# Optimization experiments

Hardware: AMD Instinct MI355X
Metric: run time of the kernel (lower is better)

## Reference

```python
import jax, jax.numpy as jnp
import numpy as np

B, N, N_HEAD, HDIM = 16, 512, 8, 64


def setup_inputs() -> dict:
    key = jax.random.key(0)
    kq, kk, kv, kg = jax.random.split(key, 4)
    q = jax.random.normal(kq, (B, N, N_HEAD, HDIM), dtype=jnp.float32)
    k = jax.random.normal(kk, (B, N, N_HEAD, HDIM), dtype=jnp.float32)
    v = jax.random.normal(kv, (B, N, N_HEAD, HDIM), dtype=jnp.float32)
    geo_f = jax.random.normal(kg, (B, N, N), dtype=jnp.float32)
    return {"q": q, "k": k, "v": v, "geo_f": geo_f}


def reference(q, k, v, geo_f):
    # q,k,v: [B,N,H,D]; geo_f: [B,N,N]
    D = q.shape[-1]
    scale = D ** (-0.5)  # total_weight = qk_weight / scale  (i.e. * sqrt(D))
    # pairwise_distance = negative squared Euclidean distance between per-head
    # query/key vectors: -||q_i - k_j||^2 = 2 q.k - ||q||^2 - ||k||^2
    qk = jnp.einsum('bnhd,bmhd->bhnm', q, k)            # [B,H,N,N]
    q2 = jnp.sum(q * q, axis=-1).transpose(0, 2, 1)     # [B,H,N]
    k2 = jnp.sum(k * k, axis=-1).transpose(0, 2, 1)     # [B,H,N]
    dist = 2.0 * qk - q2[..., :, None] - k2[..., None, :]
    total = (dist + geo_f[:, None, :, :]) / scale       # geo bias broadcast over heads
    # global max subtraction in the source is a no-op under softmax; softmax is stable anyway
    w = jax.nn.softmax(total, axis=-1)                  # [B,H,N,N]
    # weighted sum over keys m (dropout p=0.0 -> identity)
    out = jnp.einsum('bmhd,bhnm->bnhd', v, w)           # [B,N,H,D]
    return out
```

## Files before the change

### kernel.cpp

```cpp
#include <hip/hip_runtime.h>
#include <hip/hip_bf16.h>

#define BB 16
#define NN 512
#define NH 8
#define DD 64
#define CK 64
#define NCH 8
#define TL 4
#define MWAVES 8
#define MQBLK 128
#define QBLK 64
#define WAVES 4
#define KBLK 128
#define NCHUNK 4
#define NT 32
#define TPC 8

typedef __attribute__((ext_vector_type(8))) short bf16x8;
typedef __attribute__((ext_vector_type(4))) float f32x4;

__device__ __forceinline__ unsigned short f2bf(float f) {
    unsigned int u = __float_as_uint(f);
    u += 0x7fffu + ((u >> 16) & 1u);
    return (unsigned short)(u >> 16);
}
__device__ __forceinline__ float bf2f(unsigned short h) {
    return __uint_as_float(((unsigned int)h) << 16);
}
__device__ __forceinline__ void gload16(const void* gsrc, void* lds) {
    __builtin_amdgcn_global_load_lds(
        (const __attribute__((address_space(1))) unsigned int*)gsrc,
        (__attribute__((address_space(3))) unsigned int*)lds, 16, 0, 0);
}

__global__ __launch_bounds__(256) void geo_prep(
    const float* __restrict__ K, const float* __restrict__ V,
    unsigned short* __restrict__ KhiG, unsigned short* __restrict__ KloG,
    unsigned short* __restrict__ VtG, float* __restrict__ k2G)
{
    const int c2 = blockIdx.x;
    const int h  = blockIdx.y;
    const int b  = blockIdx.z;
    const int bh = b*NH + h;
    const int tid = threadIdx.x;
    const int lane16 = tid & 15;
    const int grp    = tid >> 4;

    __shared__ unsigned short Vl[DD*66];

    const size_t kbase = (size_t)bh*(NN*DD) + (size_t)c2*(CK*DD);
    #pragma unroll
    for (int kk = 0; kk < 4; ++kk) {
        const int kl = kk*16 + grp;
        const float* krow = K + ((size_t)(((b*NN + c2*CK + kl)*NH) + h))*DD + lane16*4;
        const float* vrow = V + ((size_t)(((b*NN + c2*CK + kl)*NH) + h))*DD + lane16*4;
        float4 kf = *(const float4*)krow;
        float4 vf = *(const float4*)vrow;
        float fb[4] = {kf.x, kf.y, kf.z, kf.w};
        float vb[4] = {vf.x, vf.y, vf.z, vf.w};
        unsigned short hu[4], lu[4];
        float k2s = 0.f;
        #pragma unroll
        for (int e = 0; e < 4; ++e) {
            float f = fb[e];
            k2s += f*f;
            hu[e] = f2bf(f);
            lu[e] = f2bf(f - bf2f(hu[e]));
            Vl[(lane16*4 + e)*66 + kl] = f2bf(vb[e]);
        }
        k2s += __shfl_xor(k2s, 1);
        k2s += __shfl_xor(k2s, 2);
        k2s += __shfl_xor(k2s, 4);
        k2s += __shfl_xor(k2s, 8);
        if (lane16 == 0) k2G[bh*NN + c2*CK + kl] = k2s;
        const int pos = (kl*DD + lane16*4) ^ ((kl & 7) << 3);
        *(uint2*)&KhiG[kbase + pos] = make_uint2((unsigned)hu[0] | ((unsigned)hu[1] << 16),
                                                 (unsigned)hu[2] | ((unsigned)hu[3] << 16));
        *(uint2*)&KloG[kbase + pos] = make_uint2((unsigned)lu[0] | ((unsigned)lu[1] << 16),
                                                 (unsigned)lu[2] | ((unsigned)lu[3] << 16));
    }
    __syncthreads();
    const size_t vbase = ((size_t)bh*NCH + c2)*(DD*CK);
    #pragma unroll
    for (int i = 0; i < 4; ++i) {
        const int gi = tid + 256*i;
        const int d   = gi >> 4;
        const int kl4 = (gi & 15) * 4;
        unsigned short e0 = Vl[d*66 + kl4+0];
        unsigned short e1 = Vl[d*66 + kl4+1];
        unsigned short e2 = Vl[d*66 + kl4+2];
        unsigned short e3 = Vl[d*66 + kl4+3];
        const int pos = (d*CK + kl4) ^ ((d & 7) << 3);
        *(uint2*)&VtG[vbase + pos] = make_uint2((unsigned)e0 | ((unsigned)e1 << 16),
                                                (unsigned)e2 | ((unsigned)e3 << 16));
    }
}

__global__ __launch_bounds__(512, 4) void geo_attn_main(
    const float* __restrict__ Q, const float* __restrict__ GEO,
    const unsigned short* __restrict__ KhiG, const unsigned short* __restrict__ KloG,
    const unsigned short* __restrict__ VtG, const float* __restrict__ k2G,
    float* __restrict__ OUT)
{
    const int bid  = blockIdx.x;
    const int tile = (bid & 7) * 64 + (bid >> 3);
    const int qt = tile & 3;
    const int h  = (tile >> 2) & 7;
    const int b  = tile >> 5;
    const int bh = b*NH + h;
    const int tid = threadIdx.x;
    const int w    = tid >> 6;
    const int lane = tid & 63;
    const int g = lane >> 4;
    const int c = lane & 15;

    __shared__ unsigned short Khi[2][CK*DD];
    __shared__ unsigned short Klo[2][CK*DD];
    __shared__ unsigned short vT [2][CK*DD];
    __shared__ unsigned short Pld[MWAVES*16*CK];
    __shared__ float k2s[NN];
    __shared__ float sRow[MWAVES][16];
    __shared__ float rowinv[MWAVES][16];

    if (tid < NN) k2s[tid] = k2G[(size_t)bh*NN + tid];

    const int qb = qt*MQBLK + w*16;

    bf16x8 qhi[2], qlo[2];
    float q2v = 0.f;
    {
        const float* qrow = Q + ((size_t)((b*NN + qb + c)*NH + h))*DD;
        #pragma unroll
        for (int dc = 0; dc < 2; ++dc) {
            float buf[8];
            *(float4*)&buf[0] = *(const float4*)(qrow + dc*32 + g*8);
            *(float4*)&buf[4] = *(const float4*)(qrow + dc*32 + g*8 + 4);
            #pragma unroll
            for (int i = 0; i < 8; ++i) {
                float f = buf[i];
                q2v += f*f;
                unsigned short hu = f2bf(f);
                qhi[dc][i] = (short)hu;
                qlo[dc][i] = (short)f2bf(f - bf2f(hu));
            }
        }
    }
    q2v += __shfl_xor(q2v, 16);
    q2v += __shfl_xor(q2v, 32);
    float nq2[4];
    #pragma unroll
    for (int r = 0; r < 4; ++r) nq2[r] = -8.f * __shfl(q2v, g*4 + r);

    f32x4 oacc[4];
    #pragma unroll
    for (int cb = 0; cb < 4; ++cb) { oacc[cb][0]=0.f; oacc[cb][1]=0.f; oacc[cb][2]=0.f; oacc[cb][3]=0.f; }
    float m_r[4] = {-3e38f, -3e38f, -3e38f, -3e38f};
    float l_r[4] = {0.f, 0.f, 0.f, 0.f};

    const char* gKhiB = (const char*)KhiG + (size_t)bh*(NN*DD*2);
    const char* gKloB = (const char*)KloG + (size_t)bh*(NN*DD*2);
    const char* gVtB  = (const char*)VtG  + (size_t)bh*(NN*DD*2);

    auto stage = [&](int buf, int ch2) {
        const int off = w*1024 + (lane<<4);
        gload16(gKhiB + ch2*(CK*DD*2) + off, (char*)&Khi[buf][0] + w*1024);
        gload16(gKloB + ch2*(CK*DD*2) + off, (char*)&Klo[buf][0] + w*1024);
        gload16(gVtB  + ch2*(CK*DD*2) + off, (char*)&vT [buf][0] + w*1024);
    };

    stage(0, 0);
    __syncthreads();

    for (int ch = 0; ch < NCH; ++ch) {
        const int cur = ch & 1;
        if (ch + 1 < NCH) stage(cur ^ 1, ch + 1);

        float greg[16];
        {
            const float* gb2 = GEO + (size_t)b*NN*NN + (size_t)(qb + 4*g)*NN + ch*CK + c;
            #pragma unroll
            for (int tl = 0; tl < TL; ++tl)
                #pragma unroll
                for (int r = 0; r < 4; ++r)
                    greg[tl*4+r] = gb2[(size_t)r*NN + tl*16];
        }

        f32x4 sacc[TL];
        #pragma unroll
        for (int tl = 0; tl < TL; ++tl) { sacc[tl][0]=0.f; sacc[tl][1]=0.f; sacc[tl][2]=0.f; sacc[tl][3]=0.f; }
        __builtin_amdgcn_s_setprio(1);
        #pragma unroll
        for (int tl = 0; tl < TL; ++tl) {
            const int key = tl*16 + c;
            #pragma unroll
            for (int dc = 0; dc < 2; ++dc) {
                const int idx = (key*DD + dc*32 + g*8) ^ ((key & 7) << 3);
                bf16x8 kh = *(const bf16x8*)&Khi[cur][idx];
                bf16x8 kl = *(const bf16x8*)&Klo[cur][idx];
                sacc[tl] = __builtin_amdgcn_mfma_f32_16x16x32_bf16(qhi[dc], kh, sacc[tl], 0,0,0);
                sacc[tl] = __builtin_amdgcn_mfma_f32_16x16x32_bf16(qlo[dc], kh, sacc[tl], 0,0,0);
                sacc[tl] = __builtin_amdgcn_mfma_f32_16x16x32_bf16(qhi[dc], kl, sacc[tl], 0,0,0);
            }
        }
        __builtin_amdgcn_s_setprio(0);

        float cmax[4] = {-3e38f, -3e38f, -3e38f, -3e38f};
        #pragma unroll
        for (int tl = 0; tl < TL; ++tl) {
            const float kk8 = -8.f * k2s[ch*CK + tl*16 + c];
            #pragma unroll
            for (int r = 0; r < 4; ++r) {
                float s = fmaf(16.f, sacc[tl][r], fmaf(8.f, greg[tl*4+r], nq2[r] + kk8));
                sacc[tl][r] = s;
                cmax[r] = fmaxf(cmax[r], s);
            }
        }
        float fac[4];
        #pragma unroll
        for (int r = 0; r < 4; ++r) {
            float mv = cmax[r];
            mv = fmaxf(mv, __shfl_xor(mv, 1));
            mv = fmaxf(mv, __shfl_xor(mv, 2));
            mv = fmaxf(mv, __shfl_xor(mv, 4));
            mv = fmaxf(mv, __shfl_xor(mv, 8));
            const float mnew = fmaxf(m_r[r], mv);
            fac[r] = __expf(m_r[r] - mnew);
            m_r[r] = mnew;
        }
        if (c == 0) {
            #pragma unroll
            for (int r = 0; r < 4; ++r) sRow[w][4*g + r] = fac[r];
        }
        #pragma unroll
        for (int r = 0; r < 4; ++r) l_r[r] *= fac[r];
        #pragma unroll
        for (int tl = 0; tl < TL; ++tl) {
            #pragma unroll
            for (int r = 0; r < 4; ++r) {
                float p = __expf(sacc[tl][r] - m_r[r]);
                l_r[r] += p;
                const int qloc = 4*g + r;
                Pld[(((w*16 + qloc)*CK) + tl*16 + c) ^ ((qloc & 7) << 3)] = f2bf(p);
            }
        }
        __syncthreads();

        const float sc = sRow[w][c];
        #pragma unroll
        for (int cb = 0; cb < 4; ++cb) {
            oacc[cb][0] *= sc; oacc[cb][1] *= sc; oacc[cb][2] *= sc; oacc[cb][3] *= sc;
        }
        __builtin_amdgcn_s_setprio(1);
        #pragma unroll
        for (int kc = 0; kc < 2; ++kc) {
            bf16x8 pf = *(const bf16x8*)&Pld[(((w*16 + c)*CK) + kc*32 + g*8) ^ ((c & 7) << 3)];
            #pragma unroll
            for (int cb = 0; cb < 4; ++cb) {
                const int d = cb*16 + c;
                bf16x8 vfr = *(const bf16x8*)&vT[cur][(d*CK + kc*32 + g*8) ^ ((d & 7) << 3)];
                oacc[cb] = __builtin_amdgcn_mfma_f32_16x16x32_bf16(vfr, pf, oacc[cb], 0,0,0);
            }
        }
        __builtin_amdgcn_s_setprio(0);
        __syncthreads();
    }

    #pragma unroll
    for (int r = 0; r < 4; ++r) {
        float sv = l_r[r];
        sv += __shfl_xor(sv, 1);
        sv += __shfl_xor(sv, 2);
        sv += __shfl_xor(sv, 4);
        sv += __shfl_xor(sv, 8);
        if (c == 0) rowinv[w][4*g + r] = 1.f / sv;
    }
    __syncthreads();
    const float inv = rowinv[w][c];
    float* orow = OUT + ((size_t)((b*NN + qb + c)*NH + h))*DD + 4*g;
    #pragma unroll
    for (int cb = 0; cb < 4; ++cb) {
        float4 ov;
        ov.x = oacc[cb][0] * inv;
        ov.y = oacc[cb][1] * inv;
        ov.z = oacc[cb][2] * inv;
        ov.w = oacc[cb][3] * inv;
        *(float4*)(orow + cb*16) = ov;
    }
}

__global__ __launch_bounds__(256, 2) void geo_attn_fallback(
    const float* __restrict__ Q, const float* __restrict__ K,
    const float* __restrict__ V, const float* __restrict__ GEO,
    float* __restrict__ OUT)
{
    const int qt  = blockIdx.x;
    const int h   = blockIdx.y;
    const int b   = blockIdx.z;
    const int tid = threadIdx.x;
    const int w    = tid >> 6;
    const int lane = tid & 63;
    const int g = lane >> 4;
    const int c = lane & 15;

    __shared__ unsigned short smemA[16384];
    __shared__ float k2p[2][NN];
    __shared__ float rowinvF[WAVES][16];

    unsigned short* KhiF = smemA;
    unsigned short* KloF = smemA + KBLK*DD;
    unsigned short* vTF  = smemA;
    unsigned short* PldF = smemA + DD*KBLK + w*16*KBLK;

    const int qb = qt*QBLK + w*16;

    bf16x8 qhi[2], qlo[2];
    float q2v = 0.f;
    {
        const float* qrow = Q + ((size_t)((b*NN + qb + c)*NH + h))*DD;
        #pragma unroll
        for (int dc = 0; dc < 2; ++dc) {
            float buf[8];
            *(float4*)&buf[0] = *(const float4*)(qrow + dc*32 + g*8);
            *(float4*)&buf[4] = *(const float4*)(qrow + dc*32 + g*8 + 4);
            #pragma unroll
            for (int i = 0; i < 8; ++i) {
                float f = buf[i];
                q2v += f*f;
                unsigned short hu = f2bf(f);
                qhi[dc][i] = (short)hu;
                qlo[dc][i] = (short)f2bf(f - bf2f(hu));
            }
        }
    }
    q2v += __shfl_xor(q2v, 16);
    q2v += __shfl_xor(q2v, 32);

    f32x4 zero4; zero4[0]=0.f; zero4[1]=0.f; zero4[2]=0.f; zero4[3]=0.f;
    f32x4 acc[NT];
    #pragma unroll
    for (int t = 0; t < NT; ++t) acc[t] = zero4;

    #pragma unroll
    for (int c2 = 0; c2 < NCHUNK; ++c2) {
        __syncthreads();
        {
            const int keyl = tid & (KBLK-1);
            const int half = tid >> 7;
            const int d0 = half*32;
            const float* krow = K + ((size_t)((b*NN + c2*KBLK + keyl)*NH + h))*DD + d0;
            float k2sv = 0.f;
            #pragma unroll
            for (int jj = 0; jj < 8; ++jj) {
                float4 f4 = *(const float4*)(krow + jj*4);
                float fb[4] = {f4.x, f4.y, f4.z, f4.w};
                unsigned short hu[4], lu[4];
                #pragma unroll
                for (int e = 0; e < 4; ++e) {
                    float f = fb[e];
                    k2sv += f*f;
                    hu[e] = f2bf(f);
                    lu[e] = f2bf(f - bf2f(hu[e]));
                }
                int idx = (keyl*DD + d0 + jj*4) ^ ((keyl & 7) << 3);
                *(uint2*)&KhiF[idx] = make_uint2((unsigned)hu[0] | ((unsigned)hu[1] << 16),
                                                 (unsigned)hu[2] | ((unsigned)hu[3] << 16));
                *(uint2*)&KloF[idx] = make_uint2((unsigned)lu[0] | ((unsigned)lu[1] << 16),
                                                 (unsigned)lu[2] | ((unsigned)lu[3] << 16));
            }
            k2p[half][c2*KBLK + keyl] = k2sv;
        }
        __syncthreads();
        #pragma unroll
        for (int tl = 0; tl < TPC; ++tl) {
            const int key = tl*16 + c;
            #pragma unroll
            for (int dc = 0; dc < 2; ++dc) {
                int idx = (key*DD + dc*32 + g*8) ^ ((key & 7) << 3);
                bf16x8 kh = *(const bf16x8*)&KhiF[idx];
                bf16x8 kl = *(const bf16x8*)&KloF[idx];
                acc[c2*TPC+tl] = __builtin_amdgcn_mfma_f32_16x16x32_bf16(qhi[dc], kh, acc[c2*TPC+tl], 0,0,0);
                acc[c2*TPC+tl] = __builtin_amdgcn_mfma_f32_16x16x32_bf16(qlo[dc], kh, acc[c2*TPC+tl], 0,0,0);
                acc[c2*TPC+tl] = __builtin_amdgcn_mfma_f32_16x16x32_bf16(qhi[dc], kl, acc[c2*TPC+tl], 0,0,0);
            }
        }
    }

    float nq2[4];
    #pragma unroll
    for (int r = 0; r < 4; ++r) nq2[r] = -8.f * __shfl(q2v, g*4 + r);

    const float* geoB = GEO + (size_t)b*NN*NN + (size_t)(qb + 4*g)*NN;

    float mx[4] = {-3e38f, -3e38f, -3e38f, -3e38f};
    #pragma unroll
    for (int t = 0; t < NT; ++t) {
        float kk8 = -8.f * (k2p[0][t*16 + c] + k2p[1][t*16 + c]);
        #pragma unroll
        for (int r = 0; r < 4; ++r) {
            float gv = geoB[(size_t)r*NN + t*16 + c];
            float s = fmaf(16.f, acc[t][r], fmaf(8.f, gv, nq2[r] + kk8));
            acc[t][r] = s;
            mx[r] = fmaxf(mx[r], s);
        }
    }
    #pragma unroll
    for (int r = 0; r < 4; ++r) {
        float mv = mx[r];
        mv = fmaxf(mv, __shfl_xor(mv, 1));
        mv = fmaxf(mv, __shfl_xor(mv, 2));
        mv = fmaxf(mv, __shfl_xor(mv, 4));
        mv = fmaxf(mv, __shfl_xor(mv, 8));
        mx[r] = mv;
    }
    float sm[4] = {0.f, 0.f, 0.f, 0.f};
    #pragma unroll
    for (int t = 0; t < NT; ++t) {
        #pragma unroll
        for (int r = 0; r < 4; ++r) {
            float p = __expf(acc[t][r] - mx[r]);
            acc[t][r] = p;
            sm[r] += p;
        }
    }
    #pragma unroll
    for (int r = 0; r < 4; ++r) {
        float sv = sm[r];
        sv += __shfl_xor(sv, 1);
        sv += __shfl_xor(sv, 2);
        sv += __shfl_xor(sv, 4);
        sv += __shfl_xor(sv, 8);
        sm[r] = sv;
    }
    if (c == 0) {
        #pragma unroll
        for (int r = 0; r < 4; ++r) rowinvF[w][4*g + r] = 1.f / sm[r];
    }

    f32x4 oacc[4];
    #pragma unroll
    for (int cb = 0; cb < 4; ++cb) oacc[cb] = zero4;

    #pragma unroll
    for (int c2 = 0; c2 < NCHUNK; ++c2) {
        __syncthreads();
        {
            const int keyl = tid & (KBLK-1);
            const int half = tid >> 7;
            const int d0 = half*32;
            const float* vrow = V + ((size_t)((b*NN + c2*KBLK + keyl)*NH + h))*DD + d0;
            #pragma unroll
            for (int jj = 0; jj < 8; ++jj) {
                float4 f4 = *(const float4*)(vrow + jj*4);
                float fb[4] = {f4.x, f4.y, f4.z, f4.w};
                #pragma unroll
                for (int e = 0; e < 4; ++e) {
                    int d = d0 + jj*4 + e;
                    vTF[(d*KBLK + keyl) ^ ((d & 7) << 3)] = f2bf(fb[e]);
                }
            }
        }
        #pragma unroll
        for (int tl = 0; tl < TPC; ++tl) {
            #pragma unroll
            for (int r = 0; r < 4; ++r) {
                int qloc = 4*g + r;
                PldF[(qloc*KBLK + tl*16 + c) ^ ((qloc & 7) << 3)] = f2bf(acc[c2*TPC+tl][r]);
            }
        }
        __syncthreads();
        #pragma unroll
        for (int kc = 0; kc < 4; ++kc) {
            int kb2 = kc*32 + g*8;
            bf16x8 pf = *(const bf16x8*)&PldF[(c*KBLK + kb2) ^ ((c & 7) << 3)];
            #pragma unroll
            for (int cb = 0; cb < 4; ++cb) {
                int d = cb*16 + c;
                bf16x8 vf = *(const bf16x8*)&vTF[(d*KBLK + kb2) ^ ((d & 7) << 3)];
                oacc[cb] = __builtin_amdgcn_mfma_f32_16x16x32_bf16(vf, pf, oacc[cb], 0,0,0);
            }
        }
    }

    const float inv = rowinvF[w][c];
    float* orow = OUT + ((size_t)((b*NN + qb + c)*NH + h))*DD + 4*g;
    #pragma unroll
    for (int cb = 0; cb < 4; ++cb) {
        float4 ov;
        ov.x = oacc[cb][0] * inv;
        ov.y = oacc[cb][1] * inv;
        ov.z = oacc[cb][2] * inv;
        ov.w = oacc[cb][3] * inv;
        *(float4*)(orow + cb*16) = ov;
    }
}

extern "C" void kernel_launch(void* const* d_in, const int* in_sizes, int n_in,
                              void* d_out, int out_size, void* d_ws, size_t ws_size,
                              hipStream_t stream) {
    const float* q   = (const float*)d_in[0];
    const float* k   = (const float*)d_in[1];
    const float* v   = (const float*)d_in[2];
    const float* geo = (const float*)d_in[3];
    float* out = (float*)d_out;

    const size_t IMG = (size_t)BB*NH*NN*DD*2;
    const size_t need = 3*IMG + (size_t)BB*NH*NN*4;

    if (ws_size >= need) {
        unsigned short* KhiG = (unsigned short*)d_ws;
        unsigned short* KloG = (unsigned short*)((char*)d_ws + IMG);
        unsigned short* VtG  = (unsigned short*)((char*)d_ws + 2*IMG);
        float*          k2G  = (float*)((char*)d_ws + 3*IMG);
        dim3 pgrid(NCH, NH, BB);
        geo_prep<<<pgrid, 256, 0, stream>>>(k, v, KhiG, KloG, VtG, k2G);
        geo_attn_main<<<dim3(512), 512, 0, stream>>>(q, geo, KhiG, KloG, VtG, k2G, out);
    } else {
        dim3 grid(NN/QBLK, NH, BB);
        geo_attn_fallback<<<grid, 256, 0, stream>>>(q, k, v, geo, out);
    }
}
```

Baseline: 144.1 us.

## Transpose QK MFMA so each lane owns one query row, dropping cross-lane softmax shuffles

Swaps the MFMA operand order so the score tile comes out transposed, which gives each lane a single query row. The online-softmax max and sum then need only two shuffles, and the shared-memory exchange of rescale factors and row inverses goes away along with one __syncthreads per chunk. It also drops the q-norm term, which cancels under softmax, folds the -8 factor into the precomputed k2, loads geo bias as float4 vectors, and packs P to bf16 with v_cvt_pk_bf16_f32 for wider LDS stores. In exchange it relies on the intra-wave ordering of the P writes and reads without a block barrier.

```diff
diff --git a/kernel.cpp b/kernel.cpp
--- a/kernel.cpp
+++ b/kernel.cpp
@@ -28,6 +28,11 @@
 __device__ __forceinline__ float bf2f(unsigned short h) {
     return __uint_as_float(((unsigned int)h) << 16);
 }
+__device__ __forceinline__ unsigned int cvtpk(float a, float b) {
+    unsigned int r;
+    asm("v_cvt_pk_bf16_f32 %0, %1, %2" : "=v"(r) : "v"(a), "v"(b));
+    return r;
+}
 __device__ __forceinline__ void gload16(const void* gsrc, void* lds) {
     __builtin_amdgcn_global_load_lds(
         (const __attribute__((address_space(1))) unsigned int*)gsrc,
@@ -73,7 +78,7 @@
         k2s += __shfl_xor(k2s, 2);
         k2s += __shfl_xor(k2s, 4);
         k2s += __shfl_xor(k2s, 8);
-        if (lane16 == 0) k2G[bh*NN + c2*CK + kl] = k2s;
+        if (lane16 == 0) k2G[bh*NN + c2*CK + kl] = -8.f * k2s;
         const int pos = (kl*DD + lane16*4) ^ ((kl & 7) << 3);
         *(uint2*)&KhiG[kbase + pos] = make_uint2((unsigned)hu[0] | ((unsigned)hu[1] << 16),
                                                  (unsigned)hu[2] | ((unsigned)hu[3] << 16));
@@ -119,16 +124,13 @@
     __shared__ unsigned short Klo[2][CK*DD];
     __shared__ unsigned short vT [2][CK*DD];
     __shared__ unsigned short Pld[MWAVES*16*CK];
-    __shared__ float k2s[NN];
-    __shared__ float sRow[MWAVES][16];
-    __shared__ float rowinv[MWAVES][16];
-
-    if (tid < NN) k2s[tid] = k2G[(size_t)bh*NN + tid];
+    __shared__ float k2n[NN];
+
+    if (tid < NN) k2n[tid] = k2G[(size_t)bh*NN + tid];
 
     const int qb = qt*MQBLK + w*16;
 
     bf16x8 qhi[2], qlo[2];
-    float q2v = 0.f;
     {
         const float* qrow = Q + ((size_t)((b*NN + qb + c)*NH + h))*DD;
         #pragma unroll
@@ -139,28 +141,23 @@
             #pragma unroll
             for (int i = 0; i < 8; ++i) {
                 float f = buf[i];
-                q2v += f*f;
                 unsigned short hu = f2bf(f);
                 qhi[dc][i] = (short)hu;
                 qlo[dc][i] = (short)f2bf(f - bf2f(hu));
             }
         }
     }
-    q2v += __shfl_xor(q2v, 16);
-    q2v += __shfl_xor(q2v, 32);
-    float nq2[4];
-    #pragma unroll
-    for (int r = 0; r < 4; ++r) nq2[r] = -8.f * __shfl(q2v, g*4 + r);
 
     f32x4 oacc[4];
     #pragma unroll
     for (int cb = 0; cb < 4; ++cb) { oacc[cb][0]=0.f; oacc[cb][1]=0.f; oacc[cb][2]=0.f; oacc[cb][3]=0.f; }
-    float m_r[4] = {-3e38f, -3e38f, -3e38f, -3e38f};
-    float l_r[4] = {0.f, 0.f, 0.f, 0.f};
+    float m_run = -3e38f;
+    float l_run = 0.f;
 
     const char* gKhiB = (const char*)KhiG + (size_t)bh*(NN*DD*2);
     const char* gKloB = (const char*)KloG + (size_t)bh*(NN*DD*2);
     const char* gVtB  = (const char*)VtG  + (size_t)bh*(NN*DD*2);
+    const float* geoR = GEO + (size_t)b*NN*NN + (size_t)(qb + c)*NN;
 
     auto stage = [&](int buf, int ch2) {
         const int off = w*1024 + (lane<<4);
@@ -174,17 +171,18 @@
 
     for (int ch = 0; ch < NCH; ++ch) {
         const int cur = ch & 1;
+
+        float4 gq[TL];
+        #pragma unroll
+        for (int tl = 0; tl < TL; ++tl)
+            gq[tl] = *(const float4*)(geoR + ch*CK + tl*16 + 4*g);
+
         if (ch + 1 < NCH) stage(cur ^ 1, ch + 1);
 
-        float greg[16];
-        {
-            const float* gb2 = GEO + (size_t)b*NN*NN + (size_t)(qb + 4*g)*NN + ch*CK + c;
-            #pragma unroll
-            for (int tl = 0; tl < TL; ++tl)
-                #pragma unroll
-                for (int r = 0; r < 4; ++r)
-                    greg[tl*4+r] = gb2[(size_t)r*NN + tl*16];
-        }
+        float4 kn[TL];
+        #pragma unroll
+        for (int tl = 0; tl < TL; ++tl)
+            kn[tl] = *(const float4*)&k2n[ch*CK + tl*16 + 4*g];
 
         f32x4 sacc[TL];
         #pragma unroll
@@ -198,58 +196,49 @@
                 const int idx = (key*DD + dc*32 + g*8) ^ ((key & 7) << 3);
                 bf16x8 kh = *(const bf16x8*)&Khi[cur][idx];
                 bf16x8 kl = *(const bf16x8*)&Klo[cur][idx];
-                sacc[tl] = __builtin_amdgcn_mfma_f32_16x16x32_bf16(qhi[dc], kh, sacc[tl], 0,0,0);
-                sacc[tl] = __builtin_amdgcn_mfma_f32_16x16x32_bf16(qlo[dc], kh, sacc[tl], 0,0,0);
-                sacc[tl] = __builtin_amdgcn_mfma_f32_16x16x32_bf16(qhi[dc], kl, sacc[tl], 0,0,0);
+                sacc[tl] = __builtin_amdgcn_mfma_f32_16x16x32_bf16(kh, qhi[dc], sacc[tl], 0,0,0);
+                sacc[tl] = __builtin_amdgcn_mfma_f32_16x16x32_bf16(kh, qlo[dc], sacc[tl], 0,0,0);
+                sacc[tl] = __builtin_amdgcn_mfma_f32_16x16x32_bf16(kl, qhi[dc], sacc[tl], 0,0,0);
             }
         }
         __builtin_amdgcn_s_setprio(0);
 
-        float cmax[4] = {-3e38f, -3e38f, -3e38f, -3e38f};
+        float p[16];
+        float cmax = -3e38f;
         #pragma unroll
         for (int tl = 0; tl < TL; ++tl) {
-            const float kk8 = -8.f * k2s[ch*CK + tl*16 + c];
+            const float ge[4] = {gq[tl].x, gq[tl].y, gq[tl].z, gq[tl].w};
+            const float ke[4] = {kn[tl].x, kn[tl].y, kn[tl].z, kn[tl].w};
             #pragma unroll
             for (int r = 0; r < 4; ++r) {
-                float s = fmaf(16.f, sacc[tl][r], fmaf(8.f, greg[tl*4+r], nq2[r] + kk8));
-                sacc[tl][r] = s;
-                cmax[r] = fmaxf(cmax[r], s);
-            }
-        }
-        float fac[4];
-        #pragma unroll
-        for (int r = 0; r < 4; ++r) {
-            float mv = cmax[r];
-            mv = fmaxf(mv, __shfl_xor(mv, 1));
-            mv = fmaxf(mv, __shfl_xor(mv, 2));
-            mv = fmaxf(mv, __shfl_xor(mv, 4));
-            mv = fmaxf(mv, __shfl_xor(mv, 8));
-            const float mnew = fmaxf(m_r[r], mv);
-            fac[r] = __expf(m_r[r] - mnew);
-            m_r[r] = mnew;
-        }
-        if (c == 0) {
-            #pragma unroll
-            for (int r = 0; r < 4; ++r) sRow[w][4*g + r] = fac[r];
-        }
-        #pragma unroll
-        for (int r = 0; r < 4; ++r) l_r[r] *= fac[r];
+                float s = fmaf(16.f, sacc[tl][r], fmaf(8.f, ge[r], ke[r]));
+                p[tl*4+r] = s;
+                cmax = fmaxf(cmax, s);
+            }
+        }
+        cmax = fmaxf(cmax, __shfl_xor(cmax, 16));
+        cmax = fmaxf(cmax, __shfl_xor(cmax, 32));
+        const float mnew = fmaxf(m_run, cmax);
+        const float fac = __expf(m_run - mnew);
+        m_run = mnew;
+        float cs = 0.f;
+        #pragma unroll
+        for (int i = 0; i < 16; ++i) { p[i] = __expf(p[i] - mnew); cs += p[i]; }
+        cs += __shfl_xor(cs, 16);
+        cs += __shfl_xor(cs, 32);
+        l_run = fmaf(l_run, fac, cs);
+
         #pragma unroll
         for (int tl = 0; tl < TL; ++tl) {
-            #pragma unroll
-            for (int r = 0; r < 4; ++r) {
-                float p = __expf(sacc[tl][r] - m_r[r]);
-                l_r[r] += p;
-                const int qloc = 4*g + r;
-                Pld[(((w*16 + qloc)*CK) + tl*16 + c) ^ ((qloc & 7) << 3)] = f2bf(p);
-            }
-        }
-        __syncthreads();
-
-        const float sc = sRow[w][c];
+            unsigned int u0 = cvtpk(p[tl*4+0], p[tl*4+1]);
+            unsigned int u1 = cvtpk(p[tl*4+2], p[tl*4+3]);
+            const int idx = (((w*16 + c)*CK) + tl*16 + 4*g) ^ ((c & 7) << 3);
+            *(uint2*)&Pld[idx] = make_uint2(u0, u1);
+        }
+
         #pragma unroll
         for (int cb = 0; cb < 4; ++cb) {
-            oacc[cb][0] *= sc; oacc[cb][1] *= sc; oacc[cb][2] *= sc; oacc[cb][3] *= sc;
+            oacc[cb][0] *= fac; oacc[cb][1] *= fac; oacc[cb][2] *= fac; oacc[cb][3] *= fac;
         }
         __builtin_amdgcn_s_setprio(1);
         #pragma unroll
@@ -266,17 +255,7 @@
         __syncthreads();
     }
 
-    #pragma unroll
-    for (int r = 0; r < 4; ++r) {
-        float sv = l_r[r];
-        sv += __shfl_xor(sv, 1);
-        sv += __shfl_xor(sv, 2);
-        sv += __shfl_xor(sv, 4);
-        sv += __shfl_xor(sv, 8);
-        if (c == 0) rowinv[w][4*g + r] = 1.f / sv;
-    }
-    __syncthreads();
-    const float inv = rowinv[w][c];
+    const float inv = 1.f / l_run;
     float* orow = OUT + ((size_t)((b*NN + qb + c)*NH + h))*DD + 4*g;
     #pragma unroll
     for (int cb = 0; cb < 4; ++cb) {
```

New measurement: 132.8 us. 7.8% less time.
